# Kernel tuning notes

Measured on AMD Instinct MI355X. Metric: run time of the kernel, lower is better.

## Reference

```python
import jax, jax.numpy as jnp
import numpy as np

N, E = 50000, 800000          # nodes, edges (avg degree 16)
D_IN, D_H, D_OUT = 128, 128, 64
BN_EPS = 1e-5


def setup_inputs() -> dict:
    key = jax.random.key(0)
    ks = jax.random.split(key, 8)
    g = lambda k, shp, s: jax.random.normal(k, shp, jnp.float32) * s
    return {
        "x": jax.random.normal(ks[0], (N, D_IN), jnp.float32),
        "edge_index": jax.random.randint(ks[1], (2, E), 0, N),
        # SAGEConv layer 1: lin_l (neighbors, with bias), lin_r (root, no bias)
        "Wl1": g(ks[2], (D_IN, D_H), 0.05),
        "Wr1": g(ks[3], (D_IN, D_H), 0.05),
        "b1": jnp.zeros((D_H,), jnp.float32),
        # BatchNorm1d(hidden)
        "gamma": jnp.ones((D_H,), jnp.float32),
        "beta": jnp.zeros((D_H,), jnp.float32),
        # SAGEConv layer 2
        "Wl2": g(ks[4], (D_H, D_OUT), 0.05),
        "Wr2": g(ks[5], (D_H, D_OUT), 0.05),
        "b2": jnp.zeros((D_OUT,), jnp.float32),
    }


def _sage_conv(x, src, dst, Wl, Wr, b):
    """PyG SAGEConv (mean aggr): lin_l(mean_{j in N(i)} x_j) + lin_r(x_i)."""
    n = x.shape[0]
    agg = jax.ops.segment_sum(x[src], dst, num_segments=n)            # [N, d]
    cnt = jax.ops.segment_sum(jnp.ones((src.shape[0],), x.dtype), dst,
                              num_segments=n)                          # [N]
    agg = agg / jnp.maximum(cnt, 1.0)[:, None]                         # mean, 0 for isolated
    return agg @ Wl + x @ Wr + b


def _batch_norm(x, gamma, beta):
    """Training-mode BatchNorm1d: batch stats over the node axis, biased var."""
    mu = jnp.mean(x, axis=0)
    var = jnp.var(x, axis=0)
    return gamma * (x - mu) * jax.lax.rsqrt(var + BN_EPS) + beta


def reference(x, edge_index, Wl1, Wr1, b1, gamma, beta, Wl2, Wr2, b2):
    src, dst = edge_index[0], edge_index[1]
    h = _sage_conv(x, src, dst, Wl1, Wr1, b1)
    h = jax.nn.relu(_batch_norm(h, gamma, beta))
    # dropout is identity in eval / deterministic reference
    return _sage_conv(h, src, dst, Wl2, Wr2, b2)
```

## Files before the change

### kernel.cpp

```cpp
#include <hip/hip_runtime.h>
#include <hip/hip_bf16.h>
#include <hip/hip_fp8.h>

#define DIN   128
#define DH    128
#define DOUTC 64
#define BN_EPS 1e-5f

typedef __attribute__((ext_vector_type(8))) short bf16x8;
typedef __attribute__((ext_vector_type(4))) float f32x4;
typedef __attribute__((ext_vector_type(2))) float f32x2;

#ifndef __has_builtin
#define __has_builtin(x) 0
#endif
#if __has_builtin(__builtin_amdgcn_cvt_pk_f32_fp8) && __has_builtin(__builtin_amdgcn_cvt_pk_fp8_f32)
#define HW_FP8 1
#else
#define HW_FP8 0
#endif

__device__ inline unsigned short f2bf(float f) {
    __hip_bfloat16 b = __float2bfloat16(f);
    return *reinterpret_cast<unsigned short*>(&b);
}
__device__ inline float bf2f(unsigned short u) {
    return __uint_as_float(((unsigned int)u) << 16);
}

__device__ inline void fp8x4_to_f32(unsigned int w, float* o) {
#if HW_FP8
    f32x2 lo = __builtin_amdgcn_cvt_pk_f32_fp8((int)w, false);
    f32x2 hi = __builtin_amdgcn_cvt_pk_f32_fp8((int)w, true);
    o[0] = lo.x; o[1] = lo.y; o[2] = hi.x; o[3] = hi.y;
#else
    #pragma unroll
    for (int c = 0; c < 4; ++c) {
        __hip_fp8_e4m3 q; q.__x = (__hip_fp8_storage_t)((w >> (8 * c)) & 0xFF);
        o[c] = (float)q;
    }
#endif
}
__device__ inline unsigned int f32x4_to_fp8(float a, float b, float c, float d) {
#if HW_FP8
    int p = __builtin_amdgcn_cvt_pk_fp8_f32(a, b, 0, false);
    p = __builtin_amdgcn_cvt_pk_fp8_f32(c, d, p, true);
    return (unsigned int)p;
#else
    __hip_fp8_e4m3 qa(a), qb(b), qc(c), qd(d);
    return (unsigned int)qa.__x | ((unsigned int)qb.__x << 8) |
           ((unsigned int)qc.__x << 16) | ((unsigned int)qd.__x << 24);
#endif
}

__device__ inline void block_excl_scan_256(const int* __restrict__ arr,
                                           int* __restrict__ excl,
                                           int* __restrict__ wsum, int tid)
{
    int lane = tid & 63, w = tid >> 6;
    int v = arr[tid];
    int inc = v;
    #pragma unroll
    for (int off = 1; off < 64; off <<= 1) {
        int t = __shfl_up(inc, off, 64);
        if (lane >= off) inc += t;
    }
    if (lane == 63) wsum[w] = inc;
    __syncthreads();
    if (tid == 0) {
        int s = 0;
        #pragma unroll
        for (int i = 0; i < 4; ++i) { int t = wsum[i]; wsum[i] = s; s += t; }
    }
    __syncthreads();
    excl[tid] = inc - v + wsum[w];
    __syncthreads();
}

__global__ __launch_bounds__(256) void cvtpack_kernel(
    const float* __restrict__ x, unsigned short* __restrict__ xb,
    unsigned char* __restrict__ xq,
    const float* __restrict__ Wl1, const float* __restrict__ Wr1,
    const float* __restrict__ Wl2, const float* __restrict__ Wr2,
    unsigned short* __restrict__ W1p, unsigned short* __restrict__ W2p,
    int total8, int cvt_blocks)
{
    int b = blockIdx.x;
    if (b < cvt_blocks) {
        int i = b * 256 + threadIdx.x;
        if (i >= total8) return;
        float4 a = ((const float4*)x)[2 * i];
        float4 c = ((const float4*)x)[2 * i + 1];
        unsigned short t[8];
        t[0]=f2bf(a.x); t[1]=f2bf(a.y); t[2]=f2bf(a.z); t[3]=f2bf(a.w);
        t[4]=f2bf(c.x); t[5]=f2bf(c.y); t[6]=f2bf(c.z); t[7]=f2bf(c.w);
        *(uint4*)(xb + (size_t)i * 8) = *(uint4*)t;
        uint2 pk;
        pk.x = f32x4_to_fp8(a.x, a.y, a.z, a.w);
        pk.y = f32x4_to_fp8(c.x, c.y, c.z, c.w);
        *(uint2*)(xq + (size_t)i * 8) = pk;
    } else {
        int region = (b - cvt_blocks) >> 6;
        int idx = ((b - cvt_blocks) & 63) * 256 + threadIdx.x;
        int k = idx >> 7, c = idx & 127;
        int d = ((k >> 5) * 8 + (c >> 4)) * 512 + ((k >> 3) & 3) * 128 + (c & 15) * 8 + (k & 7);
        if (region == 0) {
            W1p[d] = f2bf(Wl1[idx]);
        } else if (region == 1) {
            W1p[128 * 128 + d] = f2bf(Wr1[idx]);
        } else {
            float v = (c < 64) ? Wl2[k * 64 + c] : Wr2[k * 64 + (c - 64)];
            W2p[d] = f2bf(v);
        }
    }
}

__global__ __launch_bounds__(256) void bin_coarse(
    const int* __restrict__ ei, int* __restrict__ cursor,
    unsigned int* __restrict__ coarse, int E, int nb, int cap)
{
    __shared__ int hist[256], lstart[256], gbase[256], wsum[4];
    __shared__ unsigned int staged[4096];
    const int tid = threadIdx.x;
    const int chunkBase = blockIdx.x * 4096;

    hist[tid] = 0;
    __syncthreads();

    unsigned int rec[16]; int pos[16]; int bb[16];
    #pragma unroll
    for (int i = 0; i < 16; ++i) {
        int e = chunkBase + i * 256 + tid;
        if (e < E) {
            int s = ei[e], d = ei[E + e];
            rec[i] = ((unsigned int)d << 16) | (unsigned int)s;
            bb[i]  = d >> 8;
            pos[i] = atomicAdd(&hist[bb[i]], 1);
        } else bb[i] = -1;
    }
    __syncthreads();

    block_excl_scan_256(hist, lstart, wsum, tid);

    if (tid < nb) {
        int c = hist[tid];
        gbase[tid] = c ? atomicAdd(&cursor[tid], c) : 0;
    }
    __syncthreads();

    #pragma unroll
    for (int i = 0; i < 16; ++i)
        if (bb[i] >= 0) staged[lstart[bb[i]] + pos[i]] = rec[i];
    __syncthreads();

    int total = min(4096, E - chunkBase);
    for (int i = tid; i < total; i += 256) {
        unsigned int r = staged[i];
        int b   = (int)(r >> 24);
        int gp  = gbase[b] + (i - lstart[b]);
        if (gp < cap) coarse[(size_t)b * cap + gp] = r;
    }
}

__global__ __launch_bounds__(256) void bin_fine(
    const int* __restrict__ cursor, const unsigned int* __restrict__ coarse,
    unsigned short* __restrict__ sorted, int* __restrict__ deg,
    int* __restrict__ row_start, int n, int cap)
{
    __shared__ int hist[256], pstart[256], cur2[256], wsum[4];
    const int b = blockIdx.x, tid = threadIdx.x;
    const int cnt = min(cursor[b], cap);
    const unsigned int* src = coarse + (size_t)b * cap;

    hist[tid] = 0;
    __syncthreads();

    int nIter = (cnt + 255) >> 8;
    for (int i = 0; i < nIter; ++i) {
        int idx = i * 256 + tid;
        if (idx < cnt) atomicAdd(&hist[(src[idx] >> 16) & 255], 1);
    }
    __syncthreads();

    block_excl_scan_256(hist, pstart, wsum, tid);
    cur2[tid] = pstart[tid];
    __syncthreads();

    for (int i = 0; i < nIter; ++i) {
        int idx = i * 256 + tid;
        if (idx < cnt) {
            unsigned int r = src[idx];
            int dl = (r >> 16) & 255;
            int p  = atomicAdd(&cur2[dl], 1);
            sorted[(size_t)b * cap + p] = (unsigned short)(r & 0xFFFFu);
        }
    }

    int node = b * 256 + tid;
    if (node < n) {
        deg[node]       = hist[tid];
        row_start[node] = b * cap + pstart[tid];
    }
}

__global__ __launch_bounds__(256) void agg_gather128(
    const int* __restrict__ row_start, const int* __restrict__ deg,
    const unsigned short* __restrict__ sorted, const unsigned char* __restrict__ xq,
    unsigned short* __restrict__ aggb, int n)
{
    int wave = (blockIdx.x * 256 + threadIdx.x) >> 6;
    int lane = threadIdx.x & 63;
    if (wave >= n) return;
    int sub = lane & 7;
    int oct = lane >> 3;
    int base = row_start[wave];
    int d    = deg[wave];
    float acc[16];
    #pragma unroll
    for (int j = 0; j < 16; ++j) acc[j] = 0.f;

    for (int k0 = 0; k0 < d; k0 += 64) {
        int idx = k0 + lane;
        int mys = (idx < d) ? (int)sorted[base + idx] : 0;
        int kmax = min(64, d - k0);
        int ko   = kmax & ~7;
        for (int k = 0; k < ko; k += 8) {
            int s = __shfl(mys, k + oct, 64);
            uint4 raw = ((const uint4*)(xq + (size_t)s * DIN))[sub];
            const unsigned int* w = (const unsigned int*)&raw;
            #pragma unroll
            for (int c = 0; c < 4; ++c) {
                float o4[4];
                fp8x4_to_f32(w[c], o4);
                acc[c*4+0] += o4[0]; acc[c*4+1] += o4[1];
                acc[c*4+2] += o4[2]; acc[c*4+3] += o4[3];
            }
        }
        int rem = kmax - ko;
        if (rem) {
            int srcl = ko + oct;
            if (srcl >= kmax) srcl = kmax - 1;
            int s = __shfl(mys, srcl, 64);
            if (oct < rem) {
                uint4 raw = ((const uint4*)(xq + (size_t)s * DIN))[sub];
                const unsigned int* w = (const unsigned int*)&raw;
                #pragma unroll
                for (int c = 0; c < 4; ++c) {
                    float o4[4];
                    fp8x4_to_f32(w[c], o4);
                    acc[c*4+0] += o4[0]; acc[c*4+1] += o4[1];
                    acc[c*4+2] += o4[2]; acc[c*4+3] += o4[3];
                }
            }
        }
    }
    #pragma unroll
    for (int j = 0; j < 16; ++j) {
        acc[j] += __shfl_xor(acc[j], 32, 64);
        acc[j] += __shfl_xor(acc[j], 16, 64);
        acc[j] += __shfl_xor(acc[j],  8, 64);
    }
    if (oct == 0) {
        float inv = 1.0f / fmaxf((float)d, 1.0f);
        unsigned short t[16];
        #pragma unroll
        for (int j = 0; j < 16; ++j) t[j] = f2bf(acc[j] * inv);
        unsigned short* op = aggb + (size_t)wave * DIN + sub * 16;
        *(uint4*)op = ((uint4*)t)[0];
        *(uint4*)(op + 8) = ((uint4*)t)[1];
    }
}

__global__ __launch_bounds__(256) void agg_gather64_add(
    const int* __restrict__ row_start, const int* __restrict__ deg,
    const unsigned short* __restrict__ sorted, const unsigned short* __restrict__ P,
    float* __restrict__ out, int n)
{
    int wave = (blockIdx.x * 256 + threadIdx.x) >> 6;
    int lane = threadIdx.x & 63;
    if (wave >= n) return;
    int sub = lane & 7;
    int oct = lane >> 3;
    int base = row_start[wave];
    int d    = deg[wave];
    float acc[8];
    #pragma unroll
    for (int j = 0; j < 8; ++j) acc[j] = 0.f;

    for (int k0 = 0; k0 < d; k0 += 64) {
        int idx = k0 + lane;
        int mys = (idx < d) ? (int)sorted[base + idx] : 0;
        int kmax = min(64, d - k0);
        int ko   = kmax & ~7;
        for (int k = 0; k < ko; k += 8) {
            int s = __shfl(mys, k + oct, 64);
            uint4 raw = ((const uint4*)(P + (size_t)s * DOUTC))[sub];
            const unsigned short* u = (const unsigned short*)&raw;
            #pragma unroll
            for (int j = 0; j < 8; ++j) acc[j] += bf2f(u[j]);
        }
        int rem = kmax - ko;
        if (rem) {
            int srcl = ko + oct;
            if (srcl >= kmax) srcl = kmax - 1;
            int s = __shfl(mys, srcl, 64);
            if (oct < rem) {
                uint4 raw = ((const uint4*)(P + (size_t)s * DOUTC))[sub];
                const unsigned short* u = (const unsigned short*)&raw;
                #pragma unroll
                for (int j = 0; j < 8; ++j) acc[j] += bf2f(u[j]);
            }
        }
    }
    #pragma unroll
    for (int j = 0; j < 8; ++j) {
        acc[j] += __shfl_xor(acc[j], 32, 64);
        acc[j] += __shfl_xor(acc[j], 16, 64);
        acc[j] += __shfl_xor(acc[j],  8, 64);
    }
    if (oct == 0) {
        float inv = 1.0f / fmaxf((float)d, 1.0f);
        float* op = out + (size_t)wave * DOUTC + sub * 8;
        float4 c0 = *(float4*)op;
        float4 c1 = *((float4*)op + 1);
        c0.x += acc[0] * inv; c0.y += acc[1] * inv;
        c0.z += acc[2] * inv; c0.w += acc[3] * inv;
        c1.x += acc[4] * inv; c1.y += acc[5] * inv;
        c1.z += acc[6] * inv; c1.w += acc[7] * inv;
        *(float4*)op = c0;
        *((float4*)op + 1) = c1;
    }
}

__global__ __launch_bounds__(256) void gemm1_mfma(
    const unsigned short* __restrict__ aggb, const unsigned short* __restrict__ xb,
    const unsigned short* __restrict__ W1p, const float* __restrict__ bias,
    unsigned short* __restrict__ hb,
    float* __restrict__ bn_sum, float* __restrict__ bn_sumsq, int n)
{
    __shared__ union {
        unsigned short A[64][136];
        float red[2][4][128];
    } sm;

    const int block_row = blockIdx.x * 64;
    const int tid  = threadIdx.x;
    const int wave = tid >> 6;
    const int lane = tid & 63;
    const int q    = lane >> 4;
    const int m16  = lane & 15;

    f32x4 acc[8];
    #pragma unroll
    for (int nt = 0; nt < 8; ++nt) acc[nt] = (f32x4){0.f, 0.f, 0.f, 0.f};

    #pragma unroll
    for (int phase = 0; phase < 2; ++phase) {
        const unsigned short* src = phase ? xb : aggb;
        #pragma unroll
        for (int i = 0; i < 4; ++i) {
            int idx = tid + i * 256;
            int r   = idx >> 4;
            int c16 = idx & 15;
            int g   = block_row + r;
            uint4 v = {0u, 0u, 0u, 0u};
            if (g < n) v = ((const uint4*)(src + (size_t)g * DIN))[c16];
            *(uint4*)&sm.A[r][c16 * 8] = v;
        }
        __syncthreads();

        #pragma unroll
        for (int ks = 0; ks < 4; ++ks) {
            bf16x8 a = *(const bf16x8*)&sm.A[wave * 16 + m16][ks * 32 + q * 8];
            const unsigned short* wp = W1p + (size_t)(phase * 4 + ks) * 8 * 512;
            #pragma unroll
            for (int nt = 0; nt < 8; ++nt) {
                bf16x8 b = *(const bf16x8*)(wp + nt * 512 + lane * 8);
                acc[nt] = __builtin_amdgcn_mfma_f32_16x16x32_bf16(a, b, acc[nt], 0, 0, 0);
            }
        }
        __syncthreads();
    }

    float psum[8], psq[8];
    #pragma unroll
    for (int nt = 0; nt < 8; ++nt) {
        int col = nt * 16 + m16;
        float bv = bias[col];
        float s = 0.f, ssq = 0.f;
        #pragma unroll
        for (int reg = 0; reg < 4; ++reg) {
            int g = block_row + wave * 16 + q * 4 + reg;
            float v = acc[nt][reg] + bv;
            if (g < n) {
                hb[(size_t)g * DH + col] = f2bf(v);
                s += v; ssq += v * v;
            }
        }
        psum[nt] = s; psq[nt] = ssq;
    }
    #pragma unroll
    for (int nt = 0; nt < 8; ++nt) {
        psum[nt] += __shfl_xor(psum[nt], 16, 64);
        psum[nt] += __shfl_xor(psum[nt], 32, 64);
        psq[nt]  += __shfl_xor(psq[nt], 16, 64);
        psq[nt]  += __shfl_xor(psq[nt], 32, 64);
    }
    if (lane < 16) {
        #pragma unroll
        for (int nt = 0; nt < 8; ++nt) {
            sm.red[0][wave][nt * 16 + lane] = psum[nt];
            sm.red[1][wave][nt * 16 + lane] = psq[nt];
        }
    }
    __syncthreads();
    if (tid < 128) {
        float s = sm.red[0][0][tid] + sm.red[0][1][tid] +
                  sm.red[0][2][tid] + sm.red[0][3][tid];
        float ssq = sm.red[1][0][tid] + sm.red[1][1][tid] +
                    sm.red[1][2][tid] + sm.red[1][3][tid];
        atomicAdd(&bn_sum[tid], s);
        atomicAdd(&bn_sumsq[tid], ssq);
    }
}

__global__ __launch_bounds__(256) void gemm2p_mfma(
    const unsigned short* __restrict__ hb,
    const float* __restrict__ bn_sum, const float* __restrict__ bn_sumsq,
    const float* __restrict__ gamma, const float* __restrict__ beta,
    const unsigned short* __restrict__ W2p, const float* __restrict__ bias,
    unsigned short* __restrict__ P, float* __restrict__ out, int n)
{
    __shared__ unsigned short A[64][136];
    __shared__ float s_scale[128], s_shift[128];

    const int block_row = blockIdx.x * 64;
    const int tid  = threadIdx.x;
    const int wave = tid >> 6;
    const int lane = tid & 63;
    const int q    = lane >> 4;
    const int m16  = lane & 15;

    if (tid < 128) {
        float invN = 1.0f / (float)n;
        float mu  = bn_sum[tid] * invN;
        float var = bn_sumsq[tid] * invN - mu * mu;
        float sc  = gamma[tid] * rsqrtf(var + BN_EPS);
        s_scale[tid] = sc;
        s_shift[tid] = beta[tid] - mu * sc;
    }
    __syncthreads();

    #pragma unroll
    for (int i = 0; i < 4; ++i) {
        int idx = tid + i * 256;
        int r   = idx >> 4;
        int c16 = idx & 15;
        int g   = block_row + r;
        unsigned short t[8] = {0,0,0,0,0,0,0,0};
        if (g < n) {
            uint4 raw = ((const uint4*)(hb + (size_t)g * DH))[c16];
            const unsigned short* u = (const unsigned short*)&raw;
            #pragma unroll
            for (int j = 0; j < 8; ++j) {
                int col = c16 * 8 + j;
                float v = bf2f(u[j]) * s_scale[col] + s_shift[col];
                t[j] = f2bf(fmaxf(v, 0.f));
            }
        }
        *(uint4*)&A[r][c16 * 8] = *(uint4*)t;
    }
    __syncthreads();

    f32x4 acc[8];
    #pragma unroll
    for (int nt = 0; nt < 8; ++nt) acc[nt] = (f32x4){0.f, 0.f, 0.f, 0.f};

    #pragma unroll
    for (int ks = 0; ks < 4; ++ks) {
        bf16x8 a = *(const bf16x8*)&A[wave * 16 + m16][ks * 32 + q * 8];
        const unsigned short* wp = W2p + (size_t)ks * 8 * 512;
        #pragma unroll
        for (int nt = 0; nt < 8; ++nt) {
            bf16x8 b = *(const bf16x8*)(wp + nt * 512 + lane * 8);
            acc[nt] = __builtin_amdgcn_mfma_f32_16x16x32_bf16(a, b, acc[nt], 0, 0, 0);
        }
    }

    #pragma unroll
    for (int nt = 0; nt < 4; ++nt) {
        int col = nt * 16 + m16;
        #pragma unroll
        for (int reg = 0; reg < 4; ++reg) {
            int g = block_row + wave * 16 + q * 4 + reg;
            if (g < n) P[(size_t)g * DOUTC + col] = f2bf(acc[nt][reg]);
        }
    }
    #pragma unroll
    for (int nt = 4; nt < 8; ++nt) {
        int col = (nt - 4) * 16 + m16;
        float bv = bias[col];
        #pragma unroll
        for (int reg = 0; reg < 4; ++reg) {
            int g = block_row + wave * 16 + q * 4 + reg;
            if (g < n) out[(size_t)g * DOUTC + col] = acc[nt][reg] + bv;
        }
    }
}

extern "C" void kernel_launch(void* const* d_in, const int* in_sizes, int n_in,
                              void* d_out, int out_size, void* d_ws, size_t ws_size,
                              hipStream_t stream)
{
    const float* x     = (const float*)d_in[0];
    const int*   ei    = (const int*)  d_in[1];
    const float* Wl1   = (const float*)d_in[2];
    const float* Wr1   = (const float*)d_in[3];
    const float* b1    = (const float*)d_in[4];
    const float* gamma = (const float*)d_in[5];
    const float* beta  = (const float*)d_in[6];
    const float* Wl2   = (const float*)d_in[7];
    const float* Wr2   = (const float*)d_in[8];
    const float* b2    = (const float*)d_in[9];
    float*       out   = (float*)d_out;

    const int N = in_sizes[0] / DIN;
    const int E = in_sizes[1] / 2;

    const int NB  = (N + 255) >> 8;
    int cap = (E / NB) * 3 / 2 + 256;
    cap = (cap + 255) & ~255;

    float* bn_sum   = (float*)d_ws;
    float* bn_sumsq = bn_sum + DH;
    int* cursor     = (int*)(bn_sumsq + DH);
    int* deg        = cursor + 256;
    int* row_start  = deg + N;
    unsigned int* coarse   = (unsigned int*)(row_start + N);
    unsigned short* sorted = (unsigned short*)(coarse + (size_t)NB * cap);
    unsigned short* hb     = sorted + (size_t)NB * cap;
    unsigned short* aggb   = hb + (size_t)N * DH;
    unsigned short* xb     = aggb + (size_t)N * DIN;
    unsigned short* P      = xb + (size_t)N * DIN;
    unsigned short* W1p    = P + (size_t)N * DOUTC;
    unsigned short* W2p    = W1p + 256 * 128;
    unsigned char*  xq     = (unsigned char*)(W2p + 128 * 128);

    hipMemsetAsync(bn_sum, 0, (2 * DH + 256) * sizeof(float), stream);

    dim3 blk(256);
    const int binA_blocks = (E + 4095) / 4096;
    const int wave_blocks = (N + 3) / 4;
    const int gemm_blocks = (N + 63) / 64;
    const int cvt_blocks  = (N * DIN / 8 + 255) / 256;

    cvtpack_kernel<<<cvt_blocks + 192, blk, 0, stream>>>(
        x, xb, xq, Wl1, Wr1, Wl2, Wr2, W1p, W2p, N * DIN / 8, cvt_blocks);

    bin_coarse<<<binA_blocks, blk, 0, stream>>>(ei, cursor, coarse, E, NB, cap);
    bin_fine<<<NB, blk, 0, stream>>>(cursor, coarse, sorted, deg, row_start, N, cap);

    agg_gather128<<<wave_blocks, blk, 0, stream>>>(row_start, deg, sorted,
                                                   xq, aggb, N);
    gemm1_mfma<<<gemm_blocks, blk, 0, stream>>>(aggb, xb, W1p, b1, hb,
                                                bn_sum, bn_sumsq, N);

    gemm2p_mfma<<<gemm_blocks, blk, 0, stream>>>(hb, bn_sum, bn_sumsq,
                                                 gamma, beta, W2p, b2,
                                                 P, out, N);
    agg_gather64_add<<<wave_blocks, blk, 0, stream>>>(row_start, deg, sorted,
                                                      P, out, N);
}
```

Baseline: 221.3 us.

## Fuse layer-1 neighbor gather into GEMM1 and merge prep and coarse binning kernels

Moves the FP8 neighbor mean aggregation into the first MFMA GEMM kernel, writing the aggregated rows straight into shared memory. This removes the bf16 `aggb` intermediate and its global write and read. The conversion, weight packing and coarse edge binning are merged into one launch, and the layer-2 gather now handles 8 rows per wave with a serial neighbor loop. Each wave now stages only its own rows, which lets some block barriers go. The cost is less parallelism in the gather: a serial per-row loop with dependent index loads inside the GEMM kernel, and more LDS per block.

Result: faster. 214.3 us (-3.2%).

```diff
diff --git a/kernel.cpp b/kernel.cpp
--- a/kernel.cpp
+++ b/kernel.cpp
@@ -27,7 +27,6 @@
 __device__ inline float bf2f(unsigned short u) {
     return __uint_as_float(((unsigned int)u) << 16);
 }
-
 __device__ inline void fp8x4_to_f32(unsigned int w, float* o) {
 #if HW_FP8
     f32x2 lo = __builtin_amdgcn_cvt_pk_f32_fp8((int)w, false);
@@ -77,17 +76,23 @@
     __syncthreads();
 }
 
-__global__ __launch_bounds__(256) void cvtpack_kernel(
+__global__ __launch_bounds__(256) void prep_kernel(
     const float* __restrict__ x, unsigned short* __restrict__ xb,
     unsigned char* __restrict__ xq,
     const float* __restrict__ Wl1, const float* __restrict__ Wr1,
     const float* __restrict__ Wl2, const float* __restrict__ Wr2,
     unsigned short* __restrict__ W1p, unsigned short* __restrict__ W2p,
-    int total8, int cvt_blocks)
-{
-    int b = blockIdx.x;
-    if (b < cvt_blocks) {
-        int i = b * 256 + threadIdx.x;
+    const int* __restrict__ ei, int* __restrict__ cursor,
+    unsigned int* __restrict__ coarse,
+    int total8, int cvtB, int E, int nb, int cap)
+{
+    __shared__ int hist[256], lstart[256], gbase[256], wsum[4];
+    __shared__ unsigned int staged[4096];
+    const int b = blockIdx.x;
+    const int tid = threadIdx.x;
+
+    if (b < cvtB) {
+        int i = b * 256 + tid;
         if (i >= total8) return;
         float4 a = ((const float4*)x)[2 * i];
         float4 c = ((const float4*)x)[2 * i + 1];
@@ -99,31 +104,23 @@
         pk.x = f32x4_to_fp8(a.x, a.y, a.z, a.w);
         pk.y = f32x4_to_fp8(c.x, c.y, c.z, c.w);
         *(uint2*)(xq + (size_t)i * 8) = pk;
-    } else {
-        int region = (b - cvt_blocks) >> 6;
-        int idx = ((b - cvt_blocks) & 63) * 256 + threadIdx.x;
+        return;
+    }
+    if (b < cvtB + 192) {
+        int region = (b - cvtB) >> 6;
+        int idx = ((b - cvtB) & 63) * 256 + tid;
         int k = idx >> 7, c = idx & 127;
         int d = ((k >> 5) * 8 + (c >> 4)) * 512 + ((k >> 3) & 3) * 128 + (c & 15) * 8 + (k & 7);
-        if (region == 0) {
-            W1p[d] = f2bf(Wl1[idx]);
-        } else if (region == 1) {
-            W1p[128 * 128 + d] = f2bf(Wr1[idx]);
-        } else {
+        if (region == 0)      W1p[d] = f2bf(Wl1[idx]);
+        else if (region == 1) W1p[128 * 128 + d] = f2bf(Wr1[idx]);
+        else {
             float v = (c < 64) ? Wl2[k * 64 + c] : Wr2[k * 64 + (c - 64)];
             W2p[d] = f2bf(v);
         }
-    }
-}
-
-__global__ __launch_bounds__(256) void bin_coarse(
-    const int* __restrict__ ei, int* __restrict__ cursor,
-    unsigned int* __restrict__ coarse, int E, int nb, int cap)
-{
-    __shared__ int hist[256], lstart[256], gbase[256], wsum[4];
-    __shared__ unsigned int staged[4096];
-    const int tid = threadIdx.x;
-    const int chunkBase = blockIdx.x * 4096;
-
+        return;
+    }
+
+    const int chunkBase = (b - cvtB - 192) * 4096;
     hist[tid] = 0;
     __syncthreads();
 
@@ -156,9 +153,9 @@
     int total = min(4096, E - chunkBase);
     for (int i = tid; i < total; i += 256) {
         unsigned int r = staged[i];
-        int b   = (int)(r >> 24);
-        int gp  = gbase[b] + (i - lstart[b]);
-        if (gp < cap) coarse[(size_t)b * cap + gp] = r;
+        int bk  = (int)(r >> 24);
+        int gp  = gbase[bk] + (i - lstart[bk]);
+        if (gp < cap) coarse[(size_t)bk * cap + gp] = r;
     }
 }
 
@@ -203,145 +200,17 @@
     }
 }
 
-__global__ __launch_bounds__(256) void agg_gather128(
+__global__ __launch_bounds__(256) void gemm1_fused(
+    const unsigned char* __restrict__ xq, const unsigned short* __restrict__ xb,
     const int* __restrict__ row_start, const int* __restrict__ deg,
-    const unsigned short* __restrict__ sorted, const unsigned char* __restrict__ xq,
-    unsigned short* __restrict__ aggb, int n)
-{
-    int wave = (blockIdx.x * 256 + threadIdx.x) >> 6;
-    int lane = threadIdx.x & 63;
-    if (wave >= n) return;
-    int sub = lane & 7;
-    int oct = lane >> 3;
-    int base = row_start[wave];
-    int d    = deg[wave];
-    float acc[16];
-    #pragma unroll
-    for (int j = 0; j < 16; ++j) acc[j] = 0.f;
-
-    for (int k0 = 0; k0 < d; k0 += 64) {
-        int idx = k0 + lane;
-        int mys = (idx < d) ? (int)sorted[base + idx] : 0;
-        int kmax = min(64, d - k0);
-        int ko   = kmax & ~7;
-        for (int k = 0; k < ko; k += 8) {
-            int s = __shfl(mys, k + oct, 64);
-            uint4 raw = ((const uint4*)(xq + (size_t)s * DIN))[sub];
-            const unsigned int* w = (const unsigned int*)&raw;
-            #pragma unroll
-            for (int c = 0; c < 4; ++c) {
-                float o4[4];
-                fp8x4_to_f32(w[c], o4);
-                acc[c*4+0] += o4[0]; acc[c*4+1] += o4[1];
-                acc[c*4+2] += o4[2]; acc[c*4+3] += o4[3];
-            }
-        }
-        int rem = kmax - ko;
-        if (rem) {
-            int srcl = ko + oct;
-            if (srcl >= kmax) srcl = kmax - 1;
-            int s = __shfl(mys, srcl, 64);
-            if (oct < rem) {
-                uint4 raw = ((const uint4*)(xq + (size_t)s * DIN))[sub];
-                const unsigned int* w = (const unsigned int*)&raw;
-                #pragma unroll
-                for (int c = 0; c < 4; ++c) {
-                    float o4[4];
-                    fp8x4_to_f32(w[c], o4);
-                    acc[c*4+0] += o4[0]; acc[c*4+1] += o4[1];
-                    acc[c*4+2] += o4[2]; acc[c*4+3] += o4[3];
-                }
-            }
-        }
-    }
-    #pragma unroll
-    for (int j = 0; j < 16; ++j) {
-        acc[j] += __shfl_xor(acc[j], 32, 64);
-        acc[j] += __shfl_xor(acc[j], 16, 64);
-        acc[j] += __shfl_xor(acc[j],  8, 64);
-    }
-    if (oct == 0) {
-        float inv = 1.0f / fmaxf((float)d, 1.0f);
-        unsigned short t[16];
-        #pragma unroll
-        for (int j = 0; j < 16; ++j) t[j] = f2bf(acc[j] * inv);
-        unsigned short* op = aggb + (size_t)wave * DIN + sub * 16;
-        *(uint4*)op = ((uint4*)t)[0];
-        *(uint4*)(op + 8) = ((uint4*)t)[1];
-    }
-}
-
-__global__ __launch_bounds__(256) void agg_gather64_add(
-    const int* __restrict__ row_start, const int* __restrict__ deg,
-    const unsigned short* __restrict__ sorted, const unsigned short* __restrict__ P,
-    float* __restrict__ out, int n)
-{
-    int wave = (blockIdx.x * 256 + threadIdx.x) >> 6;
-    int lane = threadIdx.x & 63;
-    if (wave >= n) return;
-    int sub = lane & 7;
-    int oct = lane >> 3;
-    int base = row_start[wave];
-    int d    = deg[wave];
-    float acc[8];
-    #pragma unroll
-    for (int j = 0; j < 8; ++j) acc[j] = 0.f;
-
-    for (int k0 = 0; k0 < d; k0 += 64) {
-        int idx = k0 + lane;
-        int mys = (idx < d) ? (int)sorted[base + idx] : 0;
-        int kmax = min(64, d - k0);
-        int ko   = kmax & ~7;
-        for (int k = 0; k < ko; k += 8) {
-            int s = __shfl(mys, k + oct, 64);
-            uint4 raw = ((const uint4*)(P + (size_t)s * DOUTC))[sub];
-            const unsigned short* u = (const unsigned short*)&raw;
-            #pragma unroll
-            for (int j = 0; j < 8; ++j) acc[j] += bf2f(u[j]);
-        }
-        int rem = kmax - ko;
-        if (rem) {
-            int srcl = ko + oct;
-            if (srcl >= kmax) srcl = kmax - 1;
-            int s = __shfl(mys, srcl, 64);
-            if (oct < rem) {
-                uint4 raw = ((const uint4*)(P + (size_t)s * DOUTC))[sub];
-                const unsigned short* u = (const unsigned short*)&raw;
-                #pragma unroll
-                for (int j = 0; j < 8; ++j) acc[j] += bf2f(u[j]);
-            }
-        }
-    }
-    #pragma unroll
-    for (int j = 0; j < 8; ++j) {
-        acc[j] += __shfl_xor(acc[j], 32, 64);
-        acc[j] += __shfl_xor(acc[j], 16, 64);
-        acc[j] += __shfl_xor(acc[j],  8, 64);
-    }
-    if (oct == 0) {
-        float inv = 1.0f / fmaxf((float)d, 1.0f);
-        float* op = out + (size_t)wave * DOUTC + sub * 8;
-        float4 c0 = *(float4*)op;
-        float4 c1 = *((float4*)op + 1);
-        c0.x += acc[0] * inv; c0.y += acc[1] * inv;
-        c0.z += acc[2] * inv; c0.w += acc[3] * inv;
-        c1.x += acc[4] * inv; c1.y += acc[5] * inv;
-        c1.z += acc[6] * inv; c1.w += acc[7] * inv;
-        *(float4*)op = c0;
-        *((float4*)op + 1) = c1;
-    }
-}
-
-__global__ __launch_bounds__(256) void gemm1_mfma(
-    const unsigned short* __restrict__ aggb, const unsigned short* __restrict__ xb,
+    const unsigned short* __restrict__ sorted,
     const unsigned short* __restrict__ W1p, const float* __restrict__ bias,
     unsigned short* __restrict__ hb,
     float* __restrict__ bn_sum, float* __restrict__ bn_sumsq, int n)
 {
-    __shared__ union {
-        unsigned short A[64][136];
-        float red[2][4][128];
-    } sm;
+    __shared__ unsigned short X[64][136];
+    __shared__ unsigned short G[64][136];
+    __shared__ float red[2][4][128];
 
     const int block_row = blockIdx.x * 64;
     const int tid  = threadIdx.x;
@@ -350,36 +219,73 @@
     const int q    = lane >> 4;
     const int m16  = lane & 15;
 
+    {
+        int lr = wave * 16 + (lane >> 2);
+        int g  = block_row + lr;
+        #pragma unroll
+        for (int i = 0; i < 4; ++i) {
+            int c16 = (lane & 3) + 4 * i;
+            uint4 v = {0u, 0u, 0u, 0u};
+            if (g < n) v = ((const uint4*)(xb + (size_t)g * DIN))[c16];
+            *(uint4*)&X[lr][c16 * 8] = v;
+        }
+    }
+
+    {
+        int sub = lane & 7, oct = lane >> 3;
+        #pragma unroll
+        for (int grp = 0; grp < 2; ++grp) {
+            int lr = wave * 16 + grp * 8 + oct;
+            int g  = block_row + lr;
+            float acc[16];
+            #pragma unroll
+            for (int j = 0; j < 16; ++j) acc[j] = 0.f;
+            int d = 0;
+            if (g < n) {
+                int base = row_start[g];
+                d = deg[g];
+                for (int t = 0; t < d; ++t) {
+                    int s = (int)sorted[base + t];
+                    uint4 raw = ((const uint4*)(xq + (size_t)s * DIN))[sub];
+                    const unsigned int* w = (const unsigned int*)&raw;
+                    #pragma unroll
+                    for (int c = 0; c < 4; ++c) {
+                        float o4[4];
+                        fp8x4_to_f32(w[c], o4);
+                        acc[c*4+0] += o4[0]; acc[c*4+1] += o4[1];
+                        acc[c*4+2] += o4[2]; acc[c*4+3] += o4[3];
+                    }
+                }
+            }
+            float inv = 1.0f / fmaxf((float)d, 1.0f);
+            unsigned short t16[16];
+            #pragma unroll
+            for (int j = 0; j < 16; ++j) t16[j] = f2bf(acc[j] * inv);
+            *(uint4*)&G[lr][sub * 16]     = ((uint4*)t16)[0];
+            *(uint4*)&G[lr][sub * 16 + 8] = ((uint4*)t16)[1];
+        }
+    }
+
     f32x4 acc[8];
     #pragma unroll
     for (int nt = 0; nt < 8; ++nt) acc[nt] = (f32x4){0.f, 0.f, 0.f, 0.f};
 
     #pragma unroll
-    for (int phase = 0; phase < 2; ++phase) {
-        const unsigned short* src = phase ? xb : aggb;
-        #pragma unroll
-        for (int i = 0; i < 4; ++i) {
-            int idx = tid + i * 256;
-            int r   = idx >> 4;
-            int c16 = idx & 15;
-            int g   = block_row + r;
-            uint4 v = {0u, 0u, 0u, 0u};
-            if (g < n) v = ((const uint4*)(src + (size_t)g * DIN))[c16];
-            *(uint4*)&sm.A[r][c16 * 8] = v;
-        }
-        __syncthreads();
-
-        #pragma unroll
-        for (int ks = 0; ks < 4; ++ks) {
-            bf16x8 a = *(const bf16x8*)&sm.A[wave * 16 + m16][ks * 32 + q * 8];
-            const unsigned short* wp = W1p + (size_t)(phase * 4 + ks) * 8 * 512;
-            #pragma unroll
-            for (int nt = 0; nt < 8; ++nt) {
-                bf16x8 b = *(const bf16x8*)(wp + nt * 512 + lane * 8);
-                acc[nt] = __builtin_amdgcn_mfma_f32_16x16x32_bf16(a, b, acc[nt], 0, 0, 0);
-            }
-        }
-        __syncthreads();
+    for (int ks = 0; ks < 4; ++ks) {
+        bf16x8 ag = *(const bf16x8*)&G[wave * 16 + m16][ks * 32 + q * 8];
+        const unsigned short* wp0 = W1p + (size_t)ks * 8 * 512;
+        #pragma unroll
+        for (int nt = 0; nt < 8; ++nt) {
+            bf16x8 b = *(const bf16x8*)(wp0 + nt * 512 + lane * 8);
+            acc[nt] = __builtin_amdgcn_mfma_f32_16x16x32_bf16(ag, b, acc[nt], 0, 0, 0);
+        }
+        bf16x8 ax = *(const bf16x8*)&X[wave * 16 + m16][ks * 32 + q * 8];
+        const unsigned short* wp1 = W1p + (size_t)(4 + ks) * 8 * 512;
+        #pragma unroll
+        for (int nt = 0; nt < 8; ++nt) {
+            bf16x8 b = *(const bf16x8*)(wp1 + nt * 512 + lane * 8);
+            acc[nt] = __builtin_amdgcn_mfma_f32_16x16x32_bf16(ax, b, acc[nt], 0, 0, 0);
+        }
     }
 
     float psum[8], psq[8];
@@ -409,16 +315,14 @@
     if (lane < 16) {
         #pragma unroll
         for (int nt = 0; nt < 8; ++nt) {
-            sm.red[0][wave][nt * 16 + lane] = psum[nt];
-            sm.red[1][wave][nt * 16 + lane] = psq[nt];
+            red[0][wave][nt * 16 + lane] = psum[nt];
+            red[1][wave][nt * 16 + lane] = psq[nt];
         }
     }
     __syncthreads();
     if (tid < 128) {
-        float s = sm.red[0][0][tid] + sm.red[0][1][tid] +
-                  sm.red[0][2][tid] + sm.red[0][3][tid];
-        float ssq = sm.red[1][0][tid] + sm.red[1][1][tid] +
-                    sm.red[1][2][tid] + sm.red[1][3][tid];
+        float s = red[0][0][tid] + red[0][1][tid] + red[0][2][tid] + red[0][3][tid];
+        float ssq = red[1][0][tid] + red[1][1][tid] + red[1][2][tid] + red[1][3][tid];
         atomicAdd(&bn_sum[tid], s);
         atomicAdd(&bn_sumsq[tid], ssq);
     }
@@ -451,26 +355,26 @@
     }
     __syncthreads();
 
-    #pragma unroll
-    for (int i = 0; i < 4; ++i) {
-        int idx = tid + i * 256;
-        int r   = idx >> 4;
-        int c16 = idx & 15;
-        int g   = block_row + r;
-        unsigned short t[8] = {0,0,0,0,0,0,0,0};
-        if (g < n) {
-            uint4 raw = ((const uint4*)(hb + (size_t)g * DH))[c16];
-            const unsigned short* u = (const unsigned short*)&raw;
-            #pragma unroll
-            for (int j = 0; j < 8; ++j) {
-                int col = c16 * 8 + j;
-                float v = bf2f(u[j]) * s_scale[col] + s_shift[col];
-                t[j] = f2bf(fmaxf(v, 0.f));
+    {
+        int lr = wave * 16 + (lane >> 2);
+        int g  = block_row + lr;
+        #pragma unroll
+        for (int i = 0; i < 4; ++i) {
+            int c16 = (lane & 3) + 4 * i;
+            unsigned short t[8] = {0,0,0,0,0,0,0,0};
+            if (g < n) {
+                uint4 raw = ((const uint4*)(hb + (size_t)g * DH))[c16];
+                const unsigned short* u = (const unsigned short*)&raw;
+                #pragma unroll
+                for (int j = 0; j < 8; ++j) {
+                    int col = c16 * 8 + j;
+                    float v = bf2f(u[j]) * s_scale[col] + s_shift[col];
+                    t[j] = f2bf(fmaxf(v, 0.f));
+                }
             }
-        }
-        *(uint4*)&A[r][c16 * 8] = *(uint4*)t;
-    }
-    __syncthreads();
+            *(uint4*)&A[lr][c16 * 8] = *(uint4*)t;
+        }
+    }
 
     f32x4 acc[8];
     #pragma unroll
@@ -506,6 +410,42 @@
             if (g < n) out[(size_t)g * DOUTC + col] = acc[nt][reg] + bv;
         }
     }
+}
+
+__global__ __launch_bounds__(256) void agg_gather64_add(
+    const int* __restrict__ row_start, const int* __restrict__ deg,
+    const unsigned short* __restrict__ sorted, const unsigned short* __restrict__ P,
+    float* __restrict__ out, int n)
+{
+    int wid  = (blockIdx.x * 256 + threadIdx.x) >> 6;
+    int lane = threadIdx.x & 63;
+    int sub = lane & 7, oct = lane >> 3;
+    int r = wid * 8 + oct;
+    if (r >= n) return;
+
+    float acc[8];
+    #pragma unroll
+    for (int j = 0; j < 8; ++j) acc[j] = 0.f;
+
+    int base = row_start[r];
+    int d    = deg[r];
+    for (int t = 0; t < d; ++t) {
+        int s = (int)sorted[base + t];
+        uint4 raw = ((const uint4*)(P + (size_t)s * DOUTC))[sub];
+        const unsigned short* u = (const unsigned short*)&raw;
+        #pragma unroll
+        for (int j = 0; j < 8; ++j) acc[j] += bf2f(u[j]);
+    }
+    float inv = 1.0f / fmaxf((float)d, 1.0f);
+    float* op = out + (size_t)r * DOUTC + sub * 8;
+    float4 c0 = *(float4*)op;
+    float4 c1 = *((float4*)op + 1);
+    c0.x += acc[0] * inv; c0.y += acc[1] * inv;
+    c0.z += acc[2] * inv; c0.w += acc[3] * inv;
+    c1.x += acc[4] * inv; c1.y += acc[5] * inv;
+    c1.z += acc[6] * inv; c1.w += acc[7] * inv;
+    *(float4*)op = c0;
+    *((float4*)op + 1) = c1;
 }
 
 extern "C" void kernel_launch(void* const* d_in, const int* in_sizes, int n_in,
@@ -539,8 +479,7 @@
     unsigned int* coarse   = (unsigned int*)(row_start + N);
     unsigned short* sorted = (unsigned short*)(coarse + (size_t)NB * cap);
     unsigned short* hb     = sorted + (size_t)NB * cap;
-    unsigned short* aggb   = hb + (size_t)N * DH;
-    unsigned short* xb     = aggb + (size_t)N * DIN;
+    unsigned short* xb     = hb + (size_t)N * DH;
     unsigned short* P      = xb + (size_t)N * DIN;
     unsigned short* W1p    = P + (size_t)N * DOUTC;
     unsigned short* W2p    = W1p + 256 * 128;
@@ -549,25 +488,23 @@
     hipMemsetAsync(bn_sum, 0, (2 * DH + 256) * sizeof(float), stream);
 
     dim3 blk(256);
+    const int cvtB        = (N * DIN / 8 + 255) / 256;
     const int binA_blocks = (E + 4095) / 4096;
-    const int wave_blocks = (N + 3) / 4;
     const int gemm_blocks = (N + 63) / 64;
-    const int cvt_blocks  = (N * DIN / 8 + 255) / 256;
-
-    cvtpack_kernel<<<cvt_blocks + 192, blk, 0, stream>>>(
-        x, xb, xq, Wl1, Wr1, Wl2, Wr2, W1p, W2p, N * DIN / 8, cvt_blocks);
-
-    bin_coarse<<<binA_blocks, blk, 0, stream>>>(ei, cursor, coarse, E, NB, cap);
+    const int g64_blocks  = ((N + 7) / 8 + 3) / 4;
+
+    prep_kernel<<<cvtB + 192 + binA_blocks, blk, 0, stream>>>(
+        x, xb, xq, Wl1, Wr1, Wl2, Wr2, W1p, W2p,
+        ei, cursor, coarse, N * DIN / 8, cvtB, E, NB, cap);
+
     bin_fine<<<NB, blk, 0, stream>>>(cursor, coarse, sorted, deg, row_start, N, cap);
 
-    agg_gather128<<<wave_blocks, blk, 0, stream>>>(row_start, deg, sorted,
-                                                   xq, aggb, N);
-    gemm1_mfma<<<gemm_blocks, blk, 0, stream>>>(aggb, xb, W1p, b1, hb,
-                                                bn_sum, bn_sumsq, N);
+    gemm1_fused<<<gemm_blocks, blk, 0, stream>>>(xq, xb, row_start, deg, sorted,
+                                                 W1p, b1, hb, bn_sum, bn_sumsq, N);
 
     gemm2p_mfma<<<gemm_blocks, blk, 0, stream>>>(hb, bn_sum, bn_sumsq,
-                                                 gamma, beta, W2p, b2,
-                                                 P, out, N);
-    agg_gather64_add<<<wave_blocks, blk, 0, stream>>>(row_start, deg, sorted,
-                                                      P, out, N);
-}
+                                                 gamma, beta, W2p, b2, P, out, N);
+
+    agg_gather64_add<<<g64_blocks, blk, 0, stream>>>(row_start, deg, sorted,
+                                                     P, out, N);
+}
```
